# Kernel tuning notes

Measured on AMD Instinct MI355X. Metric: run time of the kernel, lower is better.

Reference implementation:

```python
import jax, jax.numpy as jnp
import numpy as np

SC = 30.0
M = 0.5
EPS = 1e-12  # F.normalize default eps


def _l2norm(x, axis):
    n = jnp.sqrt(jnp.sum(x * x, axis=axis, keepdims=True))
    return x / jnp.maximum(n, EPS)


def setup_inputs() -> dict:
    key = jax.random.key(0)
    k1, k2, k3, k4, k5 = jax.random.split(key, 5)
    n, in_f, out_f, books, words = 1024, 2048, 4096, 8, 256
    lw = in_f // books  # len_word = 256
    # xavier_uniform-ish scale for params
    w_lim = np.sqrt(6.0 / (out_f + lw))
    m_lim = np.sqrt(6.0 / (lw + words))
    return {
        "input": jax.random.normal(k1, (n, in_f), dtype=jnp.float32),
        "label": jax.random.randint(k2, (n,), 0, out_f, dtype=jnp.int64),
        "weight": jax.random.uniform(k3, (books, out_f, lw), jnp.float32, -w_lim, w_lim),
        "mlp": jax.random.uniform(k4, (books, lw, words), jnp.float32, -m_lim, m_lim),
        "codebooks": jax.random.normal(k5, (books, lw, words), dtype=jnp.float32),
    }


def reference(input, label, weight, mlp, codebooks):
    n, in_f = input.shape
    books, out_f, lw = weight.shape
    # split input into per-book chunks: [books, n, lw]
    x = input.reshape(n, books, lw).transpose(1, 0, 2)
    wn = _l2norm(weight, axis=2)               # [books, out_f, lw]
    xn = _l2norm(x, axis=2)                    # [books, n, lw]
    cos_xw = jnp.clip(jnp.einsum('bnd,bod->bno', xn, wn), -1.0, 1.0)  # [books,n,out_f]
    # per-book soft codeword assignment
    xc_soft = jax.nn.softmax(jnp.einsum('bnd,bdw->bnw', x, mlp), axis=2)  # [books,n,words]
    # soft-quantized features s_m: codebooks @ xc_soft^T -> [books, lw, n] -> [books, n, lw]
    s = jnp.einsum('bdw,bnw->bnd', codebooks, xc_soft)
    sn = _l2norm(s, axis=2)
    cos_sw = jnp.clip(jnp.einsum('bnd,bod->bno', sn, wn), -1.0, 1.0)
    # margin one-hot combine: oh*(cos - m) + (1-oh)*cos == cos - oh*m
    oh = jax.nn.one_hot(label, out_f, dtype=cos_xw.dtype)[None]  # [1, n, out_f]
    out1 = SC * (cos_xw - oh * M)
    out2 = SC * (cos_sw - oh * M)
    return (out1.transpose(1, 0, 2), out2.transpose(1, 0, 2), xc_soft.transpose(1, 0, 2))
```

## Files before the change

kernel.cpp:

```cpp
#include <hip/hip_runtime.h>

typedef __attribute__((ext_vector_type(8))) short short8;
typedef __attribute__((ext_vector_type(4))) float f32x4;
typedef __attribute__((ext_vector_type(8))) unsigned short u16x8;

#define BOOKS 8
#define NSAMP 1024
#define OUTF  4096
#define KDIM  256
#define OUT2_OFF 33554432ull
#define OUT3_OFF 67108864ull

__device__ __forceinline__ unsigned short f2bf(float f) {
  unsigned int u = __float_as_uint(f);
  u += 0x7fffu + ((u >> 16) & 1u);
  return (unsigned short)(u >> 16);
}
__device__ __forceinline__ float b2f(unsigned short u) {
  return __uint_as_float((unsigned)u << 16);
}

__device__ __forceinline__ float wave_sum(float v) {
  #pragma unroll
  for (int off = 32; off; off >>= 1) v += __shfl_xor(v, off, 64);
  return v;
}
__device__ __forceinline__ float qsum(float v) {
  #pragma unroll
  for (int off = 1; off < 16; off <<= 1) v += __shfl_xor(v, off, 64);
  return v;
}
__device__ __forceinline__ float qmax(float v) {
  #pragma unroll
  for (int off = 1; off < 16; off <<= 1) v = fmaxf(v, __shfl_xor(v, off, 64));
  return v;
}

__device__ __forceinline__ void gll16(const void* g, void* l) {
  __builtin_amdgcn_global_load_lds((const __attribute__((address_space(1))) void*)g,
                                   (__attribute__((address_space(3))) void*)l,
                                   16, 0, 0);
}

__global__ __launch_bounds__(256) void wnorm_kernel(const float* __restrict__ w,
                                                    unsigned short* __restrict__ wn) {
  int row  = blockIdx.x * 4 + (threadIdx.x >> 6);
  int lane = threadIdx.x & 63;
  float4 v = ((const float4*)(w + (size_t)row * KDIM))[lane];
  float ss = wave_sum(v.x*v.x + v.y*v.y + v.z*v.z + v.w*v.w);
  float inv = 1.f / fmaxf(sqrtf(ss), 1e-12f);
  ushort4 o;
  o.x = f2bf(v.x*inv); o.y = f2bf(v.y*inv); o.z = f2bf(v.z*inv); o.w = f2bf(v.w*inv);
  *(ushort4*)(wn + (size_t)row * KDIM + lane * 4) = o;
}

__global__ __launch_bounds__(256) void prep_small_kernel(const float* __restrict__ mlp,
                                                         const float* __restrict__ cb,
                                                         unsigned short* __restrict__ mlpT,
                                                         unsigned short* __restrict__ cbb) {
  int blk = blockIdx.x;
  int b = blk >> 8, d = blk & 255;
  int w = threadIdx.x;
  size_t src = ((size_t)(b * 256 + d)) * 256 + w;
  cbb[src] = f2bf(cb[src]);
  mlpT[((size_t)b * 256 + w) * 256 + d] = f2bf(mlp[src]);
}

__global__ __launch_bounds__(256) void xprep_kernel(const float* __restrict__ input,
                                                    unsigned short* __restrict__ Xb,
                                                    unsigned short* __restrict__ An) {
  int id = blockIdx.x * 4 + (threadIdx.x >> 6);
  int b = id >> 10, i = id & 1023;
  int lane = threadIdx.x & 63;
  float4 v = ((const float4*)(input + (size_t)i * 2048 + b * 256))[lane];
  float ss = wave_sum(v.x*v.x + v.y*v.y + v.z*v.z + v.w*v.w);
  float inv = 1.f / fmaxf(sqrtf(ss), 1e-12f);
  ushort4 r;
  r.x = f2bf(v.x); r.y = f2bf(v.y); r.z = f2bf(v.z); r.w = f2bf(v.w);
  *(ushort4*)(Xb + (size_t)id * KDIM + lane * 4) = r;
  ushort4 n;
  n.x = f2bf(v.x*inv); n.y = f2bf(v.y*inv); n.z = f2bf(v.z*inv); n.w = f2bf(v.w*inv);
  *(ushort4*)(An + ((size_t)b * 2048 + i) * KDIM + lane * 4) = n;
}

__global__ __launch_bounds__(256) void mid_kernel(const unsigned short* __restrict__ Xb,
                                                  const unsigned short* __restrict__ mlpT,
                                                  const unsigned short* __restrict__ cbb,
                                                  unsigned short* __restrict__ An,
                                                  float* __restrict__ out3) {
  __shared__ __align__(16) unsigned short lA[64 * 32];
  __shared__ __align__(16) unsigned short lB[256 * 32];
  __shared__ __align__(16) unsigned short lX[64 * 256];

  const int b  = blockIdx.x >> 4;
  const int m0 = (blockIdx.x & 15) * 64;
  const int tid  = threadIdx.x;
  const int wv   = tid >> 6;
  const int lane = tid & 63;
  const int r16  = lane & 15;
  const int q    = lane >> 4;

  const unsigned short* Ab = Xb   + ((size_t)b * NSAMP + m0) * KDIM;
  const unsigned short* Bm = mlpT + (size_t)b * 256 * KDIM;
  const unsigned short* Bc = cbb  + (size_t)b * 256 * KDIM;

  f32x4 acc[16];
  #pragma unroll
  for (int j = 0; j < 16; ++j) acc[j] = (f32x4){0.f, 0.f, 0.f, 0.f};

  for (int k0 = 0; k0 < KDIM; k0 += 32) {
    __syncthreads();
    { int row = tid >> 2, ko = (tid & 3) * 8;
      gll16(Ab + (size_t)row * KDIM + k0 + ko, &lA[tid * 8]); }
    #pragma unroll
    for (int c = 0; c < 4; ++c) {
      int idx = c * 256 + tid;
      int row = idx >> 2, ko = (idx & 3) * 8;
      gll16(Bm + (size_t)row * KDIM + k0 + ko, &lB[idx * 8]);
    }
    __syncthreads();
    short8 af = *(const short8*)(lA + (wv * 16 + r16) * 32 + q * 8);
    #pragma unroll
    for (int j = 0; j < 16; ++j) {
      short8 bf = *(const short8*)(lB + (j * 16 + r16) * 32 + q * 8);
      acc[j] = __builtin_amdgcn_mfma_f32_16x16x32_bf16(af, bf, acc[j], 0, 0, 0);
    }
  }

  #pragma unroll
  for (int r = 0; r < 4; ++r) {
    float mx = acc[0][r];
    #pragma unroll
    for (int j = 1; j < 16; ++j) mx = fmaxf(mx, acc[j][r]);
    mx = qmax(mx);
    float s = 0.f;
    #pragma unroll
    for (int j = 0; j < 16; ++j) { float e = __expf(acc[j][r] - mx); acc[j][r] = e; s += e; }
    s = qsum(s);
    float inv = 1.f / s;
    int row = wv * 16 + q * 4 + r;
    unsigned rb  = (unsigned)row * 512;
    unsigned msk = ((unsigned)(row & 7)) << 4;
    #pragma unroll
    for (int j = 0; j < 16; ++j) {
      unsigned byte = (rb + (unsigned)(j * 16 + r16) * 2) ^ msk;
      *(unsigned short*)((char*)lX + byte) = f2bf(acc[j][r] * inv);
    }
  }
  __syncthreads();

  #pragma unroll
  for (int p = 0; p < 8; ++p) {
    int chunk = p * 256 + tid;
    int row = chunk >> 5;
    int c8  = (chunk & 31) * 8;
    unsigned byte = ((unsigned)(row * 512 + c8 * 2)) ^ (((unsigned)(row & 7)) << 4);
    u16x8 v = *(const u16x8*)((char*)lX + byte);
    size_t o = ((size_t)(m0 + row) * 8 + b) * 256 + c8;
    float4 f0 = make_float4(b2f(v[0]), b2f(v[1]), b2f(v[2]), b2f(v[3]));
    float4 f1 = make_float4(b2f(v[4]), b2f(v[5]), b2f(v[6]), b2f(v[7]));
    *(float4*)(out3 + o)     = f0;
    *(float4*)(out3 + o + 4) = f1;
  }

  #pragma unroll
  for (int j = 0; j < 16; ++j) acc[j] = (f32x4){0.f, 0.f, 0.f, 0.f};
  for (int k0 = 0; k0 < KDIM; k0 += 32) {
    __syncthreads();
    #pragma unroll
    for (int c = 0; c < 4; ++c) {
      int idx = c * 256 + tid;
      int row = idx >> 2, ko = (idx & 3) * 8;
      gll16(Bc + (size_t)row * KDIM + k0 + ko, &lB[idx * 8]);
    }
    __syncthreads();
    int arow = wv * 16 + r16;
    unsigned abyte = ((unsigned)(arow * 512 + (k0 + q * 8) * 2)) ^ (((unsigned)(arow & 7)) << 4);
    short8 af = *(const short8*)((char*)lX + abyte);
    #pragma unroll
    for (int j = 0; j < 16; ++j) {
      short8 bf = *(const short8*)(lB + (j * 16 + r16) * 32 + q * 8);
      acc[j] = __builtin_amdgcn_mfma_f32_16x16x32_bf16(af, bf, acc[j], 0, 0, 0);
    }
  }

  #pragma unroll
  for (int r = 0; r < 4; ++r) {
    float ss = 0.f;
    #pragma unroll
    for (int j = 0; j < 16; ++j) ss += acc[j][r] * acc[j][r];
    ss = qsum(ss);
    float iv = 1.f / fmaxf(sqrtf(ss), 1e-12f);
    int row = wv * 16 + q * 4 + r;
    unsigned rb  = (unsigned)row * 512;
    unsigned msk = ((unsigned)(row & 7)) << 4;
    #pragma unroll
    for (int j = 0; j < 16; ++j) {
      unsigned byte = (rb + (unsigned)(j * 16 + r16) * 2) ^ msk;
      *(unsigned short*)((char*)lX + byte) = f2bf(acc[j][r] * iv);
    }
  }
  __syncthreads();
  #pragma unroll
  for (int p = 0; p < 8; ++p) {
    int chunk = p * 256 + tid;
    int row = chunk >> 5;
    int c8  = (chunk & 31) * 8;
    unsigned byte = ((unsigned)(row * 512 + c8 * 2)) ^ (((unsigned)(row & 7)) << 4);
    u16x8 v = *(const u16x8*)((char*)lX + byte);
    *(u16x8*)(An + ((size_t)b * 2048 + 1024 + m0 + row) * KDIM + c8) = v;
  }
}

__global__ __launch_bounds__(256) void big_gemm_kernel(const unsigned short* __restrict__ A,
                                                       const unsigned short* __restrict__ B,
                                                       float* __restrict__ Cf,
                                                       const int* __restrict__ label) {
  __shared__ __align__(16) unsigned short lA[128 * 32];
  __shared__ __align__(16) unsigned short lB[128 * 32];

  const int b  = blockIdx.z;
  const int m0 = blockIdx.y * 128;
  const int n0 = blockIdx.x * 128;
  const int tid  = threadIdx.x;
  const int wid  = tid >> 6;
  const int lane = tid & 63;
  const int wm = wid & 1, wn = wid >> 1;
  const int r16 = lane & 15;
  const int q   = lane >> 4;

  const unsigned short* Ab = A + (size_t)b * 2048 * KDIM;
  const unsigned short* Bb = B + (size_t)b * OUTF * KDIM;

  f32x4 acc[4][4];
  #pragma unroll
  for (int i = 0; i < 4; ++i)
    #pragma unroll
    for (int j = 0; j < 4; ++j) acc[i][j] = (f32x4){0.f, 0.f, 0.f, 0.f};

  for (int k0 = 0; k0 < KDIM; k0 += 32) {
    __syncthreads();
    #pragma unroll
    for (int c = 0; c < 2; ++c) {
      int idx = c * 256 + tid;
      int row = idx >> 2, ko = (idx & 3) * 8;
      gll16(Ab + (size_t)(m0 + row) * KDIM + k0 + ko, &lA[idx * 8]);
      gll16(Bb + (size_t)(n0 + row) * KDIM + k0 + ko, &lB[idx * 8]);
    }
    __syncthreads();

    short8 af[4], bfr[4];
    #pragma unroll
    for (int f = 0; f < 4; ++f) {
      af[f]  = *(const short8*)(lA + (wm * 64 + f * 16 + r16) * 32 + q * 8);
      bfr[f] = *(const short8*)(lB + (wn * 64 + f * 16 + r16) * 32 + q * 8);
    }
    #pragma unroll
    for (int i = 0; i < 4; ++i)
      #pragma unroll
      for (int j = 0; j < 4; ++j)
        acc[i][j] = __builtin_amdgcn_mfma_f32_16x16x32_bf16(af[i], bfr[j], acc[i][j], 0, 0, 0);
  }

  #pragma unroll
  for (int i = 0; i < 4; ++i) {
    int row0 = m0 + wm * 64 + i * 16 + q * 4;
    #pragma unroll
    for (int r = 0; r < 4; ++r) {
      int row = row0 + r;
      int gi  = row & 1023;
      int lb  = label[gi];
      size_t base = (size_t)(row >> 10) * OUT2_OFF + ((size_t)gi * 8 + b) * OUTF;
      #pragma unroll
      for (int j = 0; j < 4; ++j) {
        int col = n0 + wn * 64 + j * 16 + r16;
        float v = fminf(fmaxf(acc[i][j][r], -1.f), 1.f) * 30.f;
        if (col == lb) v -= 15.f;
        Cf[base + col] = v;
      }
    }
  }
}

extern "C" void kernel_launch(void* const* d_in, const int* in_sizes, int n_in,
                              void* d_out, int out_size, void* d_ws, size_t ws_size,
                              hipStream_t stream) {
  const float* input  = (const float*)d_in[0];
  const int*   label  = (const int*)d_in[1];
  const float* weight = (const float*)d_in[2];
  const float* mlp    = (const float*)d_in[3];
  const float* cb     = (const float*)d_in[4];
  float* out = (float*)d_out;

  unsigned short* wn = (unsigned short*)d_ws;
  unsigned short* An = wn + 8388608;

  unsigned short* Xb   = (unsigned short*)(out + OUT2_OFF);
  unsigned short* mlpT = Xb + 2097152;
  unsigned short* cbb  = mlpT + 524288;
  float*          out3 = out + OUT3_OFF;

  wnorm_kernel<<<dim3(8192), dim3(256), 0, stream>>>(weight, wn);
  prep_small_kernel<<<dim3(2048), dim3(256), 0, stream>>>(mlp, cb, mlpT, cbb);
  xprep_kernel<<<dim3(2048), dim3(256), 0, stream>>>(input, Xb, An);
  mid_kernel<<<dim3(128), dim3(256), 0, stream>>>(Xb, mlpT, cbb, An, out3);
  big_gemm_kernel<<<dim3(32, 16, 8), dim3(256), 0, stream>>>(An, wn, out, label);
}
```

Before: 379.8 us.

## Merge prep kernels, tile mlp transpose, remap GEMM blocks, use nontemporal stores

Three preprocessing kernels become one launch that branches on block index, which removes two launches and their gaps. The mlp transpose now goes through an LDS tile so both reads and writes are coalesced. The big GEMM remaps block indices so neighbouring blocks in launch order are spread across different row and column tiles. The large fp32 output writes in the GEMM and mid kernels use nontemporal stores to reduce cache pollution. The combined prep kernel declares a shared array for every block, which may slightly lower occupancy for the blocks that never use it.

```diff
diff --git a/kernel.cpp b/kernel.cpp
--- a/kernel.cpp
+++ b/kernel.cpp
@@ -42,45 +42,74 @@
                                    16, 0, 0);
 }
 
-__global__ __launch_bounds__(256) void wnorm_kernel(const float* __restrict__ w,
-                                                    unsigned short* __restrict__ wn) {
-  int row  = blockIdx.x * 4 + (threadIdx.x >> 6);
-  int lane = threadIdx.x & 63;
-  float4 v = ((const float4*)(w + (size_t)row * KDIM))[lane];
-  float ss = wave_sum(v.x*v.x + v.y*v.y + v.z*v.z + v.w*v.w);
-  float inv = 1.f / fmaxf(sqrtf(ss), 1e-12f);
-  ushort4 o;
-  o.x = f2bf(v.x*inv); o.y = f2bf(v.y*inv); o.z = f2bf(v.z*inv); o.w = f2bf(v.w*inv);
-  *(ushort4*)(wn + (size_t)row * KDIM + lane * 4) = o;
-}
-
-__global__ __launch_bounds__(256) void prep_small_kernel(const float* __restrict__ mlp,
-                                                         const float* __restrict__ cb,
-                                                         unsigned short* __restrict__ mlpT,
-                                                         unsigned short* __restrict__ cbb) {
-  int blk = blockIdx.x;
-  int b = blk >> 8, d = blk & 255;
-  int w = threadIdx.x;
-  size_t src = ((size_t)(b * 256 + d)) * 256 + w;
-  cbb[src] = f2bf(cb[src]);
-  mlpT[((size_t)b * 256 + w) * 256 + d] = f2bf(mlp[src]);
-}
-
-__global__ __launch_bounds__(256) void xprep_kernel(const float* __restrict__ input,
-                                                    unsigned short* __restrict__ Xb,
-                                                    unsigned short* __restrict__ An) {
-  int id = blockIdx.x * 4 + (threadIdx.x >> 6);
-  int b = id >> 10, i = id & 1023;
-  int lane = threadIdx.x & 63;
-  float4 v = ((const float4*)(input + (size_t)i * 2048 + b * 256))[lane];
-  float ss = wave_sum(v.x*v.x + v.y*v.y + v.z*v.z + v.w*v.w);
-  float inv = 1.f / fmaxf(sqrtf(ss), 1e-12f);
-  ushort4 r;
-  r.x = f2bf(v.x); r.y = f2bf(v.y); r.z = f2bf(v.z); r.w = f2bf(v.w);
-  *(ushort4*)(Xb + (size_t)id * KDIM + lane * 4) = r;
-  ushort4 n;
-  n.x = f2bf(v.x*inv); n.y = f2bf(v.y*inv); n.z = f2bf(v.z*inv); n.w = f2bf(v.w*inv);
-  *(ushort4*)(An + ((size_t)b * 2048 + i) * KDIM + lane * 4) = n;
+__global__ __launch_bounds__(256) void prep_kernel(const float* __restrict__ input,
+                                                   const float* __restrict__ weight,
+                                                   const float* __restrict__ mlp,
+                                                   const float* __restrict__ cb,
+                                                   unsigned short* __restrict__ wn,
+                                                   unsigned short* __restrict__ Xb,
+                                                   unsigned short* __restrict__ An,
+                                                   unsigned short* __restrict__ mlpT,
+                                                   unsigned short* __restrict__ cbb) {
+  __shared__ float lt[64][65];
+  const int blk = blockIdx.x;
+  const int tid = threadIdx.x;
+
+  if (blk < 8192) {
+    int row  = blk * 4 + (tid >> 6);
+    int lane = tid & 63;
+    float4 v = ((const float4*)(weight + (size_t)row * KDIM))[lane];
+    float ss = wave_sum(v.x*v.x + v.y*v.y + v.z*v.z + v.w*v.w);
+    float inv = 1.f / fmaxf(sqrtf(ss), 1e-12f);
+    ushort4 o;
+    o.x = f2bf(v.x*inv); o.y = f2bf(v.y*inv); o.z = f2bf(v.z*inv); o.w = f2bf(v.w*inv);
+    *(ushort4*)(wn + (size_t)row * KDIM + lane * 4) = o;
+  } else if (blk < 10240) {
+    int id = (blk - 8192) * 4 + (tid >> 6);
+    int b = id >> 10, i = id & 1023;
+    int lane = tid & 63;
+    float4 v = ((const float4*)(input + (size_t)i * 2048 + b * 256))[lane];
+    float ss = wave_sum(v.x*v.x + v.y*v.y + v.z*v.z + v.w*v.w);
+    float inv = 1.f / fmaxf(sqrtf(ss), 1e-12f);
+    ushort4 r;
+    r.x = f2bf(v.x); r.y = f2bf(v.y); r.z = f2bf(v.z); r.w = f2bf(v.w);
+    *(ushort4*)(Xb + (size_t)id * KDIM + lane * 4) = r;
+    ushort4 n;
+    n.x = f2bf(v.x*inv); n.y = f2bf(v.y*inv); n.z = f2bf(v.z*inv); n.w = f2bf(v.w*inv);
+    *(ushort4*)(An + ((size_t)b * 2048 + i) * KDIM + lane * 4) = n;
+  } else {
+    int t = blk - 10240;
+    int b = t >> 4, tile = t & 15;
+    int dt = (tile >> 2) * 64, wt = (tile & 3) * 64;
+    int g  = tid >> 4;
+    int l4 = (tid & 15) * 4;
+    const float* mb = mlp + (size_t)b * 256 * 256;
+    const float* cs = cb  + (size_t)b * 256 * 256;
+    #pragma unroll
+    for (int p = 0; p < 4; ++p) {
+      int d = dt + p * 16 + g;
+      float4 v = *(const float4*)(mb + (size_t)d * 256 + wt + l4);
+      lt[p * 16 + g][l4 + 0] = v.x;
+      lt[p * 16 + g][l4 + 1] = v.y;
+      lt[p * 16 + g][l4 + 2] = v.z;
+      lt[p * 16 + g][l4 + 3] = v.w;
+      float4 c = *(const float4*)(cs + (size_t)d * 256 + wt + l4);
+      ushort4 co;
+      co.x = f2bf(c.x); co.y = f2bf(c.y); co.z = f2bf(c.z); co.w = f2bf(c.w);
+      *(ushort4*)(cbb + ((size_t)(b * 256 + d)) * 256 + wt + l4) = co;
+    }
+    __syncthreads();
+    #pragma unroll
+    for (int p = 0; p < 4; ++p) {
+      int w = wt + p * 16 + g;
+      ushort4 o;
+      o.x = f2bf(lt[l4 + 0][p * 16 + g]);
+      o.y = f2bf(lt[l4 + 1][p * 16 + g]);
+      o.z = f2bf(lt[l4 + 2][p * 16 + g]);
+      o.w = f2bf(lt[l4 + 3][p * 16 + g]);
+      *(ushort4*)(mlpT + ((size_t)(b * 256 + w)) * 256 + dt + l4) = o;
+    }
+  }
 }
 
 __global__ __launch_bounds__(256) void mid_kernel(const unsigned short* __restrict__ Xb,
@@ -157,10 +186,10 @@
     unsigned byte = ((unsigned)(row * 512 + c8 * 2)) ^ (((unsigned)(row & 7)) << 4);
     u16x8 v = *(const u16x8*)((char*)lX + byte);
     size_t o = ((size_t)(m0 + row) * 8 + b) * 256 + c8;
-    float4 f0 = make_float4(b2f(v[0]), b2f(v[1]), b2f(v[2]), b2f(v[3]));
-    float4 f1 = make_float4(b2f(v[4]), b2f(v[5]), b2f(v[6]), b2f(v[7]));
-    *(float4*)(out3 + o)     = f0;
-    *(float4*)(out3 + o + 4) = f1;
+    f32x4 f0 = { b2f(v[0]), b2f(v[1]), b2f(v[2]), b2f(v[3]) };
+    f32x4 f1 = { b2f(v[4]), b2f(v[5]), b2f(v[6]), b2f(v[7]) };
+    __builtin_nontemporal_store(f0, (f32x4*)(out3 + o));
+    __builtin_nontemporal_store(f1, (f32x4*)(out3 + o + 4));
   }
 
   #pragma unroll
@@ -220,8 +249,10 @@
   __shared__ __align__(16) unsigned short lB[128 * 32];
 
   const int b  = blockIdx.z;
-  const int m0 = blockIdx.y * 128;
-  const int n0 = blockIdx.x * 128;
+  const int lin = blockIdx.x + (blockIdx.y << 5);
+  const int wg  = ((lin & 7) << 6) + (lin >> 3);
+  const int n0 = (wg & 31) * 128;
+  const int m0 = (wg >> 5) * 128;
   const int tid  = threadIdx.x;
   const int wid  = tid >> 6;
   const int lane = tid & 63;
@@ -276,7 +307,7 @@
         int col = n0 + wn * 64 + j * 16 + r16;
         float v = fminf(fmaxf(acc[i][j][r], -1.f), 1.f) * 30.f;
         if (col == lb) v -= 15.f;
-        Cf[base + col] = v;
+        __builtin_nontemporal_store(v, &Cf[base + col]);
       }
     }
   }
@@ -300,9 +331,8 @@
   unsigned short* cbb  = mlpT + 524288;
   float*          out3 = out + OUT3_OFF;
 
-  wnorm_kernel<<<dim3(8192), dim3(256), 0, stream>>>(weight, wn);
-  prep_small_kernel<<<dim3(2048), dim3(256), 0, stream>>>(mlp, cb, mlpT, cbb);
-  xprep_kernel<<<dim3(2048), dim3(256), 0, stream>>>(input, Xb, An);
+  prep_kernel<<<dim3(10368), dim3(256), 0, stream>>>(input, weight, mlp, cb,
+                                                     wn, Xb, An, mlpT, cbb);
   mid_kernel<<<dim3(128), dim3(256), 0, stream>>>(Xb, mlpT, cbb, An, out3);
   big_gemm_kernel<<<dim3(32, 16, 8), dim3(256), 0, stream>>>(An, wn, out, label);
 }
```

After: 373.7 us. No clear change (-1.6%).
